# Performance work log

Measured on AMD Instinct MI355X. Metric: run time of the kernel, lower is better.

Reference implementation:

```python
import jax, jax.numpy as jnp
import numpy as np

N_NODES = 50000
N_EDGES = 800000
N_GRAPHS = 256
IN_CH = 128
HID = 256
FFN = 256
OUT = 1


def xavier(key, shape):
    fan_in, fan_out = shape[0], shape[1]
    a = jnp.sqrt(6.0 / (fan_in + fan_out))
    return jax.random.uniform(key, shape, jnp.float32, -a, a)


def setup_inputs() -> dict:
    key = jax.random.key(0)
    ks = jax.random.split(key, 12)
    x = jax.random.normal(ks[0], (N_NODES, IN_CH), jnp.float32)
    edge_index = jax.random.randint(ks[1], (2, N_EDGES), 0, N_NODES, jnp.int32)
    batch = jnp.sort(jax.random.randint(ks[2], (N_NODES,), 0, N_GRAPHS, jnp.int32))
    return {
        "x": x,
        "edge_index": edge_index,
        "batch": batch,
        # GCNConv layers (glorot weight, zero bias as in PyG reset_parameters)
        "W1": xavier(ks[3], (IN_CH, HID)), "b1": jnp.zeros((HID,), jnp.float32),
        "W2": xavier(ks[4], (HID, HID)),   "b2": jnp.zeros((HID,), jnp.float32),
        "W3": xavier(ks[5], (HID, HID)),   "b3": jnp.zeros((HID,), jnp.float32),
        # FFN: Linear(HID, FFN) then final Linear(FFN, OUT)
        "Wf": xavier(ks[6], (HID, FFN)),   "bf": jnp.zeros((FFN,), jnp.float32),
        "Wo": xavier(ks[7], (FFN, OUT)),   "bo": jnp.zeros((OUT,), jnp.float32),
    }


def _gcn_norm(edge_index, n_nodes):
    # add self-loops, compute symmetric normalization D^-1/2 (A+I) D^-1/2
    loops = jnp.arange(n_nodes, dtype=edge_index.dtype)
    row = jnp.concatenate([edge_index[0], loops])
    col = jnp.concatenate([edge_index[1], loops])
    deg = jax.ops.segment_sum(jnp.ones_like(col, jnp.float32), col, num_segments=n_nodes)
    dis = jnp.where(deg > 0, jax.lax.rsqrt(jnp.maximum(deg, 1.0)), 0.0)
    norm = dis[row] * dis[col]  # [E+N]
    return row, col, norm


def _gcn_conv(x, W, b, row, col, norm, n_nodes):
    xw = x @ W                                   # [N, H]
    msg = xw[row] * norm[:, None]                # gather + scale  [E+N, H]
    out = jax.ops.segment_sum(msg, col, num_segments=n_nodes)
    return out + b


def reference(x, edge_index, batch, W1, b1, W2, b2, W3, b3, Wf, bf, Wo, bo):
    row, col, norm = _gcn_norm(edge_index, N_NODES)
    h = jax.nn.relu(_gcn_conv(x, W1, b1, row, col, norm, N_NODES))
    h = jax.nn.relu(_gcn_conv(h, W2, b2, row, col, norm, N_NODES))
    h = jax.nn.relu(_gcn_conv(h, W3, b3, row, col, norm, N_NODES))
    # global mean pool over graphs
    counts = jax.ops.segment_sum(jnp.ones((N_NODES,), jnp.float32), batch, num_segments=N_GRAPHS)
    pooled = jax.ops.segment_sum(h, batch, num_segments=N_GRAPHS) / jnp.maximum(counts, 1.0)[:, None]
    # FFN (dropout is identity in eval mode): Linear -> ReLU -> final Linear
    g = jax.nn.relu(pooled @ Wf + bf)
    out = g @ Wo + bo
    return out
```

## Files before the change

kernel.cpp:

```cpp
#include <hip/hip_runtime.h>
#include <hip/hip_bf16.h>
#include <hip/hip_fp16.h>


#define THREADS 256

typedef _Float16 f16x8 __attribute__((ext_vector_type(8)));
typedef float    f32x4 __attribute__((ext_vector_type(4)));


__global__ void degree_goff_kernel(const int* __restrict__ col, int* __restrict__ deg, int E,
                                   const int* __restrict__ batch, int* __restrict__ goff,
                                   int N, int G) {
    int i = blockIdx.x * THREADS + threadIdx.x;
    if (i < E) atomicAdd(&deg[col[i]], 1);
    if (i < N) {
        int b1 = batch[i];
        int b0 = (i == 0) ? -1 : batch[i - 1];
        for (int g = b0 + 1; g <= b1; ++g) goff[g] = i;
        if (i == N - 1) {
            for (int g = b1 + 1; g <= G; ++g) goff[g] = N;
        }
    }
}

__global__ __launch_bounds__(256) void scanA_kernel(
    const int* __restrict__ in, int* __restrict__ out, int* __restrict__ bsum,
    float* __restrict__ dis, int n) {
    __shared__ int wsum[4];
    int i0 = blockIdx.x * 1024 + threadIdx.x * 4;
    int lane = threadIdx.x & 63, wid = threadIdx.x >> 6;
    int v0 = 0, v1 = 0, v2 = 0, v3 = 0;
    if (i0 + 3 < n) {
        int4 v = *(const int4*)&in[i0];
        v0 = v.x; v1 = v.y; v2 = v.z; v3 = v.w;
    } else {
        if (i0 + 0 < n) v0 = in[i0 + 0];
        if (i0 + 1 < n) v1 = in[i0 + 1];
        if (i0 + 2 < n) v2 = in[i0 + 2];
        if (i0 + 3 < n) v3 = in[i0 + 3];
    }
    if (i0 + 0 < n) dis[i0 + 0] = rsqrtf((float)(v0 + 1));
    if (i0 + 1 < n) dis[i0 + 1] = rsqrtf((float)(v1 + 1));
    if (i0 + 2 < n) dis[i0 + 2] = rsqrtf((float)(v2 + 1));
    if (i0 + 3 < n) dis[i0 + 3] = rsqrtf((float)(v3 + 1));
    int s = v0 + v1 + v2 + v3;
    int inc = s;
    #pragma unroll
    for (int d = 1; d < 64; d <<= 1) {
        int t = __shfl_up(inc, d);
        if (lane >= d) inc += t;
    }
    if (lane == 63) wsum[wid] = inc;
    __syncthreads();
    int add = 0;
    for (int w = 0; w < wid; ++w) add += wsum[w];
    int ex = add + inc - s;
    if (i0 + 0 < n) out[i0 + 0] = ex;
    if (i0 + 1 < n) out[i0 + 1] = ex + v0;
    if (i0 + 2 < n) out[i0 + 2] = ex + v0 + v1;
    if (i0 + 3 < n) out[i0 + 3] = ex + v0 + v1 + v2;
    if (threadIdx.x == 255) bsum[blockIdx.x] = add + inc;
}

__global__ void scanB_kernel(int* __restrict__ bsum, int* __restrict__ total_slot, int nb) {
    int lane = threadIdx.x;
    int v = (lane < nb) ? bsum[lane] : 0;
    int inc = v;
    #pragma unroll
    for (int d = 1; d < 64; d <<= 1) {
        int t = __shfl_up(inc, d);
        if (lane >= d) inc += t;
    }
    if (lane < nb) bsum[lane] = inc - v;
    if (lane == 63) *total_slot = inc;
}

__global__ void csr_fill_kernel(const int* __restrict__ row, const int* __restrict__ col,
                                const int* __restrict__ offs, int* __restrict__ deg,
                                unsigned short* __restrict__ srcs, int E) {
    int e = blockIdx.x * THREADS + threadIdx.x;
    if (e < E) {
        int c = col[e];
        int old = atomicSub(&deg[c], 1);
        srcs[offs[c] + old - 1] = (unsigned short)row[e];
    }
}

__global__ void convert_kernel(
    int* __restrict__ offs, const int* __restrict__ bsum, int Nfix,
    const float* __restrict__ X, const float* __restrict__ dis,
    _Float16* __restrict__ Xs, int total8, int IC,
    const float* __restrict__ W1, _Float16* __restrict__ W1t, int k1,
    const float* __restrict__ W2, _Float16* __restrict__ W2t,
    const float* __restrict__ W3, _Float16* __restrict__ W3t) {
    int i = blockIdx.x * THREADS + threadIdx.x;
    if (i < Nfix) {
        offs[i] += bsum[i >> 10];
        return;
    }
    int j = i - Nfix;
    if (j < total8) {
        int idx = j * 8;
        int node = idx / IC;
        int ch0  = idx % IC;
        float d = dis[node];
        float4 a = *(const float4*)&X[idx];
        float4 b = *(const float4*)&X[idx + 4];
        f16x8 o;
        o[0] = (_Float16)(d * a.x); o[1] = (_Float16)(d * a.y);
        o[2] = (_Float16)(d * a.z); o[3] = (_Float16)(d * a.w);
        o[4] = (_Float16)(d * b.x); o[5] = (_Float16)(d * b.y);
        o[6] = (_Float16)(d * b.z); o[7] = (_Float16)(d * b.w);
        int sw = IC >> 3;
        int slice = ch0 / sw, within = ch0 % sw;
        *(f16x8*)&Xs[((size_t)slice * Nfix + node) * sw + within] = o;
        return;
    }
    j -= total8;
    int n1 = k1 * 256;
    if (j < n1) {
        int k = j >> 8, n = j & 255;
        W1t[n * k1 + k] = (_Float16)W1[j];
        return;
    }
    j -= n1;
    if (j < 65536) {
        int k = j >> 8, n = j & 255;
        W2t[n * 256 + k] = (_Float16)W2[j];
        return;
    }
    j -= 65536;
    if (j < 65536) {
        int k = j >> 8, n = j & 255;
        W3t[n * 256 + k] = (_Float16)W3[j];
    }
}


template<int CH>
__global__ __launch_bounds__(256) void aggregate_slice_kernel(
    const _Float16* __restrict__ X, const int* __restrict__ offs,
    const unsigned short* __restrict__ srcs, const float* __restrict__ dis,
    _Float16* __restrict__ A, int N) {
    constexpr int LPN = CH / 64;
    constexpr int NPB = 256 / LPN;
    int bid   = blockIdx.x;
    int slice = bid & 7;
    int tile  = bid >> 3;
    int node  = tile * NPB + threadIdx.x / LPN;
    if (node >= N) return;
    int lane = threadIdx.x % LPN;
    const f16x8* Xv = (const f16x8*)X + (size_t)slice * N * LPN;
    f16x8 self = Xv[(size_t)node * LPN + lane];
    float acc[8], acc2[8];
    #pragma unroll
    for (int j = 0; j < 8; ++j) { acc[j] = (float)self[j]; acc2[j] = 0.f; }
    int s = offs[node], e = offs[node + 1];
    int i = s;
    for (; i + 4 <= e; i += 4) {
        int s0 = (int)__builtin_nontemporal_load(&srcs[i]);
        int s1 = (int)__builtin_nontemporal_load(&srcs[i + 1]);
        int s2 = (int)__builtin_nontemporal_load(&srcs[i + 2]);
        int s3 = (int)__builtin_nontemporal_load(&srcs[i + 3]);
        f16x8 v0 = Xv[(size_t)s0 * LPN + lane];
        f16x8 v1 = Xv[(size_t)s1 * LPN + lane];
        f16x8 v2 = Xv[(size_t)s2 * LPN + lane];
        f16x8 v3 = Xv[(size_t)s3 * LPN + lane];
        #pragma unroll
        for (int j = 0; j < 8; ++j) {
            acc[j]  += (float)v0[j] + (float)v2[j];
            acc2[j] += (float)v1[j] + (float)v3[j];
        }
    }
    for (; i < e; ++i) {
        int s0 = (int)__builtin_nontemporal_load(&srcs[i]);
        f16x8 v0 = Xv[(size_t)s0 * LPN + lane];
        #pragma unroll
        for (int j = 0; j < 8; ++j) acc[j] += (float)v0[j];
    }
    float dn = dis[node];
    f16x8 o;
    #pragma unroll
    for (int j = 0; j < 8; ++j) o[j] = (_Float16)(dn * (acc[j] + acc2[j]));
    f16x8* Av = (f16x8*)A + (size_t)slice * N * LPN;
    __builtin_nontemporal_store(o, &Av[(size_t)node * LPN + lane]);
}


template<int K, int MODE>
__global__ __launch_bounds__(256) void gemm_as_kernel(
    const _Float16* __restrict__ A, const _Float16* __restrict__ Bt,
    const float* __restrict__ bias, const float* __restrict__ dscale,
    _Float16* __restrict__ H, float* __restrict__ pooled,
    const int* __restrict__ batch, int M) {
    constexpr int LSA = K + 40;
    constexpr int KC = K / 32;
    constexpr int SPR = K / 8;
    constexpr int SPS = K / 64;
    constexpr int SW  = K / 8;
    __shared__ _Float16 As[64 * LSA];
    int tid = threadIdx.x;
    int m0 = blockIdx.x * 64;

    {
        constexpr int RPI = 256 / SPR;
        int r_in = tid % RPI;
        int seg  = tid / RPI;
        int slice = seg / SPS, sub = seg % SPS;
        #pragma unroll
        for (int it = 0; it < 64 / RPI; ++it) {
            int r = it * RPI + r_in;
            int gr = m0 + r;
            uint4 v = make_uint4(0, 0, 0, 0);
            if (gr < M) v = *(const uint4*)&A[((size_t)slice * M + gr) * SW + sub * 8];
            *(uint4*)&As[r * LSA + seg * 8] = v;
        }
    }
    __syncthreads();

    int wid = tid >> 6, lane = tid & 63;
    int l16 = lane & 15, quad = lane >> 4;
    int wn = wid * 64;

    f32x4 acc[4][4] = {};
    const _Float16* Bbase = Bt + (size_t)(wn + l16) * K + quad * 8;

    #pragma unroll
    for (int kc = 0; kc < KC; ++kc) {
        f16x8 bh[4];
        #pragma unroll
        for (int ni = 0; ni < 4; ++ni)
            bh[ni] = *(const f16x8*)&Bbase[(size_t)(ni * 16) * K + kc * 32];
        #pragma unroll
        for (int mi = 0; mi < 4; ++mi) {
            f16x8 ah = *(const f16x8*)&As[(mi * 16 + l16) * LSA + kc * 32 + quad * 8];
            #pragma unroll
            for (int ni = 0; ni < 4; ++ni)
                acc[mi][ni] = __builtin_amdgcn_mfma_f32_16x16x32_f16(ah, bh[ni], acc[mi][ni], 0, 0, 0);
        }
    }

    #pragma unroll
    for (int mi = 0; mi < 4; ++mi) {
        int rbase = m0 + mi * 16;
        int g0 = 0, g15 = 0;
        if (MODE == 2) {
            g0  = batch[min(rbase, M - 1)];
            g15 = batch[min(rbase + 15, M - 1)];
        }
        #pragma unroll
        for (int ni = 0; ni < 4; ++ni) {
            int col = wn + ni * 16 + l16;
            float bv = bias[col];
            if (MODE == 1) {
                size_t hbase = ((size_t)(col >> 5) * M) * 32 + (col & 31);
                #pragma unroll
                for (int r = 0; r < 4; ++r) {
                    int grow = rbase + quad * 4 + r;
                    if (grow < M) {
                        float v = fmaxf(acc[mi][ni][r] + bv, 0.f) * dscale[grow];
                        H[hbase + (size_t)grow * 32] = (_Float16)v;
                    }
                }
            } else {
                if (g0 == g15) {
                    float p = 0.f;
                    #pragma unroll
                    for (int r = 0; r < 4; ++r) {
                        int grow = rbase + quad * 4 + r;
                        float v = fmaxf(acc[mi][ni][r] + bv, 0.f);
                        p += (grow < M) ? v : 0.f;
                    }
                    p += __shfl_xor(p, 16);
                    p += __shfl_xor(p, 32);
                    if (quad == 0) atomicAdd(&pooled[g0 * 256 + col], p);
                } else {
                    #pragma unroll
                    for (int r = 0; r < 4; ++r) {
                        int grow = rbase + quad * 4 + r;
                        if (grow < M) {
                            float v = fmaxf(acc[mi][ni][r] + bv, 0.f);
                            atomicAdd(&pooled[batch[grow] * 256 + col], v);
                        }
                    }
                }
            }
        }
    }
}


__global__ __launch_bounds__(256) void ffn_kernel(
    const float* __restrict__ pooled, const int* __restrict__ goff,
    const float* __restrict__ Wf, const float* __restrict__ bf,
    const float* __restrict__ Wo, const float* __restrict__ bo,
    float* __restrict__ out) {
    __shared__ float p[256];
    __shared__ float red[256];
    int g = blockIdx.x, t = threadIdx.x;
    int cnt = goff[g + 1] - goff[g];
    float inv = 1.f / (float)max(cnt, 1);
    p[t] = pooled[g * 256 + t] * inv;
    __syncthreads();
    float s = bf[t];
    #pragma unroll 8
    for (int k = 0; k < 256; ++k) s = fmaf(p[k], Wf[k * 256 + t], s);
    float gv = fmaxf(s, 0.f);
    red[t] = gv * Wo[t];
    __syncthreads();
    for (int o = 128; o > 0; o >>= 1) {
        if (t < o) red[t] += red[t + o];
        __syncthreads();
    }
    if (t == 0) out[g] = red[0] + bo[0];
}


extern "C" void kernel_launch(void* const* d_in, const int* in_sizes, int n_in,
                              void* d_out, int out_size, void* d_ws, size_t ws_size,
                              hipStream_t stream) {
    const float* x   = (const float*)d_in[0];
    const int*   ei  = (const int*)d_in[1];
    const int*   bat = (const int*)d_in[2];
    const float* W1  = (const float*)d_in[3];
    const float* b1  = (const float*)d_in[4];
    const float* W2  = (const float*)d_in[5];
    const float* b2  = (const float*)d_in[6];
    const float* W3  = (const float*)d_in[7];
    const float* b3  = (const float*)d_in[8];
    const float* Wf  = (const float*)d_in[9];
    const float* bf  = (const float*)d_in[10];
    const float* Wo  = (const float*)d_in[11];
    const float* bo  = (const float*)d_in[12];
    float* out = (float*)d_out;

    const int N  = in_sizes[2];
    const int E  = in_sizes[1] / 2;
    const int IC = in_sizes[0] / N;
    const int HID = 256;
    const int G  = out_size;
    const int* row = ei;
    const int* col = ei + E;

    char* w = (char*)d_ws;
    size_t off = 0;
    auto alloc = [&](size_t bytes) -> void* {
        void* p = w + off;
        off += (bytes + 255) & ~(size_t)255;
        return p;
    };
    int*   deg    = (int*)alloc((size_t)N * 4);
    float* pooled = (float*)alloc((size_t)G * HID * 4);
    float* dis    = (float*)alloc((size_t)N * 4);
    int*   offs   = (int*)alloc((size_t)(N + 1) * 4);
    unsigned short* srcs = (unsigned short*)alloc((size_t)E * 2);
    int*   goff   = (int*)alloc((size_t)(G + 1) * 4);
    int*   bsum   = (int*)alloc((size_t)64 * 4);
    _Float16* W1t = (_Float16*)alloc((size_t)HID * IC * 2);
    _Float16* W2t = (_Float16*)alloc((size_t)HID * HID * 2);
    _Float16* W3t = (_Float16*)alloc((size_t)HID * HID * 2);
    _Float16* Xs  = (_Float16*)alloc((size_t)N * IC * 2);
    _Float16* Ah  = (_Float16*)alloc((size_t)N * HID * 2);
    _Float16* Hs  = (_Float16*)alloc((size_t)N * HID * 2);
    (void)ws_size; (void)n_in;

    size_t zlen = (((size_t)N * 4 + 255) & ~(size_t)255) + (size_t)G * HID * 4;
    hipMemsetAsync(deg, 0, zlen, stream);

    int nb = (N + 1023) / 1024;
    degree_goff_kernel<<<(E + THREADS - 1) / THREADS, THREADS, 0, stream>>>(
        col, deg, E, bat, goff, N, G);
    scanA_kernel<<<nb, 256, 0, stream>>>(deg, offs, bsum, dis, N);
    scanB_kernel<<<1, 64, 0, stream>>>(bsum, &offs[N], nb);

    int total8 = N * IC / 8;
    int conv_total = N + total8 + IC * HID + HID * HID + HID * HID;
    convert_kernel<<<(conv_total + THREADS - 1) / THREADS, THREADS, 0, stream>>>(
        offs, bsum, N, x, dis, Xs, total8, IC, W1, W1t, IC, W2, W2t, W3, W3t);

    csr_fill_kernel<<<(E + THREADS - 1) / THREADS, THREADS, 0, stream>>>(row, col, offs, deg, srcs, E);

    int mtiles = (N + 63) / 64;
    int nt1 = (N + 127) / 128;
    aggregate_slice_kernel<128><<<nt1 * 8, 256, 0, stream>>>(Xs, offs, srcs, dis, Ah, N);
    gemm_as_kernel<128, 1><<<mtiles, 256, 0, stream>>>(Ah, W1t, b1, dis, Hs, nullptr, nullptr, N);
    int nt2 = (N + 63) / 64;
    aggregate_slice_kernel<256><<<nt2 * 8, 256, 0, stream>>>(Hs, offs, srcs, dis, Ah, N);
    gemm_as_kernel<256, 1><<<mtiles, 256, 0, stream>>>(Ah, W2t, b2, dis, Hs, nullptr, nullptr, N);
    aggregate_slice_kernel<256><<<nt2 * 8, 256, 0, stream>>>(Hs, offs, srcs, dis, Ah, N);
    gemm_as_kernel<256, 2><<<mtiles, 256, 0, stream>>>(Ah, W3t, b3, nullptr, nullptr, pooled, bat, N);

    ffn_kernel<<<G, 256, 0, stream>>>(pooled, goff, Wf, bf, Wo, bo, out);
}
```

Before: 458.4 us.

## Pad CSR neighbor lists to multiples of eight with a zero dummy node

Rounds each node's in-degree up to a multiple of 8 in the scan and fills the padding slots with index N. Row N of every feature buffer is zeroed, so the padded entries add nothing. The aggregation loop then reads 8 indices per 16-byte vector load, prefetches the next index vector, and gathers 8 rows per iteration with no tail loop. The cost is up to 7 wasted gathers per node (average degree is about 16), an extra padfill kernel, and a larger srcs buffer.

```diff
diff --git a/kernel.cpp b/kernel.cpp
--- a/kernel.cpp
+++ b/kernel.cpp
@@ -7,6 +7,7 @@
 
 typedef _Float16 f16x8 __attribute__((ext_vector_type(8)));
 typedef float    f32x4 __attribute__((ext_vector_type(4)));
+typedef unsigned short u16x8 __attribute__((ext_vector_type(8)));
 
 
 __global__ void degree_goff_kernel(const int* __restrict__ col, int* __restrict__ deg, int E,
@@ -44,6 +45,8 @@
     if (i0 + 1 < n) dis[i0 + 1] = rsqrtf((float)(v1 + 1));
     if (i0 + 2 < n) dis[i0 + 2] = rsqrtf((float)(v2 + 1));
     if (i0 + 3 < n) dis[i0 + 3] = rsqrtf((float)(v3 + 1));
+    v0 = (v0 + 7) & ~7; v1 = (v1 + 7) & ~7;
+    v2 = (v2 + 7) & ~7; v3 = (v3 + 7) & ~7;
     int s = v0 + v1 + v2 + v3;
     int inc = s;
     #pragma unroll
@@ -76,6 +79,15 @@
     if (lane == 63) *total_slot = inc;
 }
 
+__global__ void padfill_kernel(const int* __restrict__ offs, const int* __restrict__ deg,
+                               unsigned short* __restrict__ srcs, int N) {
+    int c = blockIdx.x * THREADS + threadIdx.x;
+    if (c < N) {
+        int s = offs[c] + deg[c], e = offs[c + 1];
+        for (int i = s; i < e; ++i) srcs[i] = (unsigned short)N;
+    }
+}
+
 __global__ void csr_fill_kernel(const int* __restrict__ row, const int* __restrict__ col,
                                 const int* __restrict__ offs, int* __restrict__ deg,
                                 unsigned short* __restrict__ srcs, int E) {
@@ -93,13 +105,15 @@
     _Float16* __restrict__ Xs, int total8, int IC,
     const float* __restrict__ W1, _Float16* __restrict__ W1t, int k1,
     const float* __restrict__ W2, _Float16* __restrict__ W2t,
-    const float* __restrict__ W3, _Float16* __restrict__ W3t) {
+    const float* __restrict__ W3, _Float16* __restrict__ W3t,
+    _Float16* __restrict__ Hs) {
     int i = blockIdx.x * THREADS + threadIdx.x;
     if (i < Nfix) {
         offs[i] += bsum[i >> 10];
         return;
     }
     int j = i - Nfix;
+    int Ms = Nfix + 1;
     if (j < total8) {
         int idx = j * 8;
         int node = idx / IC;
@@ -114,7 +128,7 @@
         o[6] = (_Float16)(d * b.z); o[7] = (_Float16)(d * b.w);
         int sw = IC >> 3;
         int slice = ch0 / sw, within = ch0 % sw;
-        *(f16x8*)&Xs[((size_t)slice * Nfix + node) * sw + within] = o;
+        *(f16x8*)&Xs[((size_t)slice * Ms + node) * sw + within] = o;
         return;
     }
     j -= total8;
@@ -134,6 +148,22 @@
     if (j < 65536) {
         int k = j >> 8, n = j & 255;
         W3t[n * 256 + k] = (_Float16)W3[j];
+        return;
+    }
+    j -= 65536;
+    {
+        int swx = IC >> 3;
+        int nx = 8 * swx;
+        if (j < nx) {
+            int slice = j / swx, wi = j % swx;
+            Xs[((size_t)slice * Ms + Nfix) * swx + wi] = (_Float16)0.f;
+            return;
+        }
+        j -= nx;
+        if (j < 256) {
+            int slice = j >> 5, wi = j & 31;
+            Hs[((size_t)slice * Ms + Nfix) * 32 + wi] = (_Float16)0.f;
+        }
     }
 }
 
@@ -151,39 +181,40 @@
     int node  = tile * NPB + threadIdx.x / LPN;
     if (node >= N) return;
     int lane = threadIdx.x % LPN;
-    const f16x8* Xv = (const f16x8*)X + (size_t)slice * N * LPN;
+    size_t Ms = (size_t)N + 1;
+    const f16x8* Xv = (const f16x8*)X + (size_t)slice * Ms * LPN;
     f16x8 self = Xv[(size_t)node * LPN + lane];
     float acc[8], acc2[8];
     #pragma unroll
     for (int j = 0; j < 8; ++j) { acc[j] = (float)self[j]; acc2[j] = 0.f; }
     int s = offs[node], e = offs[node + 1];
-    int i = s;
-    for (; i + 4 <= e; i += 4) {
-        int s0 = (int)__builtin_nontemporal_load(&srcs[i]);
-        int s1 = (int)__builtin_nontemporal_load(&srcs[i + 1]);
-        int s2 = (int)__builtin_nontemporal_load(&srcs[i + 2]);
-        int s3 = (int)__builtin_nontemporal_load(&srcs[i + 3]);
-        f16x8 v0 = Xv[(size_t)s0 * LPN + lane];
-        f16x8 v1 = Xv[(size_t)s1 * LPN + lane];
-        f16x8 v2 = Xv[(size_t)s2 * LPN + lane];
-        f16x8 v3 = Xv[(size_t)s3 * LPN + lane];
-        #pragma unroll
-        for (int j = 0; j < 8; ++j) {
-            acc[j]  += (float)v0[j] + (float)v2[j];
-            acc2[j] += (float)v1[j] + (float)v3[j];
-        }
-    }
-    for (; i < e; ++i) {
-        int s0 = (int)__builtin_nontemporal_load(&srcs[i]);
-        f16x8 v0 = Xv[(size_t)s0 * LPN + lane];
-        #pragma unroll
-        for (int j = 0; j < 8; ++j) acc[j] += (float)v0[j];
+    int nit = (e - s) >> 3;
+    if (nit > 0) {
+        const u16x8* ip = (const u16x8*)&srcs[s];
+        u16x8 idx = ip[0];
+        for (int it = 0; it < nit; ++it) {
+            u16x8 nxt = ip[min(it + 1, nit - 1)];
+            f16x8 v0 = Xv[(size_t)idx[0] * LPN + lane];
+            f16x8 v1 = Xv[(size_t)idx[1] * LPN + lane];
+            f16x8 v2 = Xv[(size_t)idx[2] * LPN + lane];
+            f16x8 v3 = Xv[(size_t)idx[3] * LPN + lane];
+            f16x8 v4 = Xv[(size_t)idx[4] * LPN + lane];
+            f16x8 v5 = Xv[(size_t)idx[5] * LPN + lane];
+            f16x8 v6 = Xv[(size_t)idx[6] * LPN + lane];
+            f16x8 v7 = Xv[(size_t)idx[7] * LPN + lane];
+            #pragma unroll
+            for (int j = 0; j < 8; ++j) {
+                acc[j]  += ((float)v0[j] + (float)v2[j]) + ((float)v4[j] + (float)v6[j]);
+                acc2[j] += ((float)v1[j] + (float)v3[j]) + ((float)v5[j] + (float)v7[j]);
+            }
+            idx = nxt;
+        }
     }
     float dn = dis[node];
     f16x8 o;
     #pragma unroll
     for (int j = 0; j < 8; ++j) o[j] = (_Float16)(dn * (acc[j] + acc2[j]));
-    f16x8* Av = (f16x8*)A + (size_t)slice * N * LPN;
+    f16x8* Av = (f16x8*)A + (size_t)slice * Ms * LPN;
     __builtin_nontemporal_store(o, &Av[(size_t)node * LPN + lane]);
 }
 
@@ -193,7 +224,7 @@
     const _Float16* __restrict__ A, const _Float16* __restrict__ Bt,
     const float* __restrict__ bias, const float* __restrict__ dscale,
     _Float16* __restrict__ H, float* __restrict__ pooled,
-    const int* __restrict__ batch, int M) {
+    const int* __restrict__ batch, int M, int Ms) {
     constexpr int LSA = K + 40;
     constexpr int KC = K / 32;
     constexpr int SPR = K / 8;
@@ -213,7 +244,7 @@
             int r = it * RPI + r_in;
             int gr = m0 + r;
             uint4 v = make_uint4(0, 0, 0, 0);
-            if (gr < M) v = *(const uint4*)&A[((size_t)slice * M + gr) * SW + sub * 8];
+            if (gr < M) v = *(const uint4*)&A[((size_t)slice * Ms + gr) * SW + sub * 8];
             *(uint4*)&As[r * LSA + seg * 8] = v;
         }
     }
@@ -254,7 +285,7 @@
             int col = wn + ni * 16 + l16;
             float bv = bias[col];
             if (MODE == 1) {
-                size_t hbase = ((size_t)(col >> 5) * M) * 32 + (col & 31);
+                size_t hbase = (size_t)(col >> 5) * Ms * 32 + (col & 31);
                 #pragma unroll
                 for (int r = 0; r < 4; ++r) {
                     int grow = rbase + quad * 4 + r;
@@ -340,6 +371,7 @@
     const int IC = in_sizes[0] / N;
     const int HID = 256;
     const int G  = out_size;
+    const int Ms = N + 1;
     const int* row = ei;
     const int* col = ei + E;
 
@@ -354,15 +386,15 @@
     float* pooled = (float*)alloc((size_t)G * HID * 4);
     float* dis    = (float*)alloc((size_t)N * 4);
     int*   offs   = (int*)alloc((size_t)(N + 1) * 4);
-    unsigned short* srcs = (unsigned short*)alloc((size_t)E * 2);
+    unsigned short* srcs = (unsigned short*)alloc(((size_t)E + 7 * (size_t)N + 8) * 2);
     int*   goff   = (int*)alloc((size_t)(G + 1) * 4);
     int*   bsum   = (int*)alloc((size_t)64 * 4);
     _Float16* W1t = (_Float16*)alloc((size_t)HID * IC * 2);
     _Float16* W2t = (_Float16*)alloc((size_t)HID * HID * 2);
     _Float16* W3t = (_Float16*)alloc((size_t)HID * HID * 2);
-    _Float16* Xs  = (_Float16*)alloc((size_t)N * IC * 2);
-    _Float16* Ah  = (_Float16*)alloc((size_t)N * HID * 2);
-    _Float16* Hs  = (_Float16*)alloc((size_t)N * HID * 2);
+    _Float16* Xs  = (_Float16*)alloc((size_t)Ms * IC * 2);
+    _Float16* Ah  = (_Float16*)alloc((size_t)Ms * HID * 2);
+    _Float16* Hs  = (_Float16*)alloc((size_t)Ms * HID * 2);
     (void)ws_size; (void)n_in;
 
     size_t zlen = (((size_t)N * 4 + 255) & ~(size_t)255) + (size_t)G * HID * 4;
@@ -375,21 +407,22 @@
     scanB_kernel<<<1, 64, 0, stream>>>(bsum, &offs[N], nb);
 
     int total8 = N * IC / 8;
-    int conv_total = N + total8 + IC * HID + HID * HID + HID * HID;
+    int conv_total = N + total8 + IC * HID + HID * HID + HID * HID + 8 * (IC / 8) + 256;
     convert_kernel<<<(conv_total + THREADS - 1) / THREADS, THREADS, 0, stream>>>(
-        offs, bsum, N, x, dis, Xs, total8, IC, W1, W1t, IC, W2, W2t, W3, W3t);
-
+        offs, bsum, N, x, dis, Xs, total8, IC, W1, W1t, IC, W2, W2t, W3, W3t, Hs);
+
+    padfill_kernel<<<(N + THREADS - 1) / THREADS, THREADS, 0, stream>>>(offs, deg, srcs, N);
     csr_fill_kernel<<<(E + THREADS - 1) / THREADS, THREADS, 0, stream>>>(row, col, offs, deg, srcs, E);
 
     int mtiles = (N + 63) / 64;
     int nt1 = (N + 127) / 128;
     aggregate_slice_kernel<128><<<nt1 * 8, 256, 0, stream>>>(Xs, offs, srcs, dis, Ah, N);
-    gemm_as_kernel<128, 1><<<mtiles, 256, 0, stream>>>(Ah, W1t, b1, dis, Hs, nullptr, nullptr, N);
+    gemm_as_kernel<128, 1><<<mtiles, 256, 0, stream>>>(Ah, W1t, b1, dis, Hs, nullptr, nullptr, N, Ms);
     int nt2 = (N + 63) / 64;
     aggregate_slice_kernel<256><<<nt2 * 8, 256, 0, stream>>>(Hs, offs, srcs, dis, Ah, N);
-    gemm_as_kernel<256, 1><<<mtiles, 256, 0, stream>>>(Ah, W2t, b2, dis, Hs, nullptr, nullptr, N);
+    gemm_as_kernel<256, 1><<<mtiles, 256, 0, stream>>>(Ah, W2t, b2, dis, Hs, nullptr, nullptr, N, Ms);
     aggregate_slice_kernel<256><<<nt2 * 8, 256, 0, stream>>>(Hs, offs, srcs, dis, Ah, N);
-    gemm_as_kernel<256, 2><<<mtiles, 256, 0, stream>>>(Ah, W3t, b3, nullptr, nullptr, pooled, bat, N);
+    gemm_as_kernel<256, 2><<<mtiles, 256, 0, stream>>>(Ah, W3t, b3, nullptr, nullptr, pooled, bat, N, Ms);
 
     ffn_kernel<<<G, 256, 0, stream>>>(pooled, goff, Wf, bf, Wo, bo, out);
 }
```

New measurement: 396.5 us. 13.5% less time.
